# Optimization experiments

Hardware: AMD Instinct MI355X
Metric: run time of the kernel (lower is better)

## Reference

```python
import jax, jax.numpy as jnp
import numpy as np

B, C, H, W = 8, 512, 32, 32
NH = 8
DH = C // NH
HW = H * W
LN_EPS = 1e-5
NORM_EPS = 1e-12  # torch F.normalize eps


def setup_inputs() -> dict:
    key = jax.random.key(0)
    ks = jax.random.split(key, 8)
    s = 0.02
    return {
        "x": jax.random.normal(ks[0], (B, C, H, W), dtype=jnp.float32),
        "qkv_w": jax.random.normal(ks[1], (3 * C, C), dtype=jnp.float32) * s,
        "proj_w": jax.random.normal(ks[2], (C, C), dtype=jnp.float32) * s,
        "proj_b": jnp.zeros((C,), dtype=jnp.float32),
        "temperature": jnp.ones((NH, 1, 1), dtype=jnp.float32),
        "ln_g": jnp.ones((C,), dtype=jnp.float32),
        "ln_b": jnp.zeros((C,), dtype=jnp.float32),
        "pos_embed": jax.random.normal(ks[3], (1, HW, C), dtype=jnp.float32) * s,
        "dw_w": jax.random.normal(ks[4], (C, 1, 3, 3), dtype=jnp.float32) * s,
        "dw_b": jnp.zeros((C,), dtype=jnp.float32),
        "pw_w": jax.random.normal(ks[5], (C, C, 1, 1), dtype=jnp.float32) * s,
        "pw_b": jnp.zeros((C,), dtype=jnp.float32),
    }


def _l2norm_tokens(t):
    # normalize along token axis (dim=-2), like F.normalize(t, dim=-2)
    n = jnp.sqrt(jnp.sum(t * t, axis=-2, keepdims=True))
    return t / jnp.maximum(n, NORM_EPS)


def _layernorm(t, g, b):
    mu = jnp.mean(t, axis=-1, keepdims=True)
    var = jnp.mean((t - mu) ** 2, axis=-1, keepdims=True)
    return (t - mu) * jax.lax.rsqrt(var + LN_EPS) * g + b


def _dsconv(t, dw_w, dw_b, pw_w, pw_b):
    # depthwise 3x3 SAME + pointwise 1x1, NCHW / OIHW
    y = jax.lax.conv_general_dilated(
        t, dw_w, window_strides=(1, 1), padding="SAME",
        dimension_numbers=("NCHW", "OIHW", "NCHW"), feature_group_count=C)
    y = y + dw_b[None, :, None, None]
    y = jax.lax.conv_general_dilated(
        y, pw_w, window_strides=(1, 1), padding="SAME",
        dimension_numbers=("NCHW", "OIHW", "NCHW"))
    return y + pw_b[None, :, None, None]


def reference(x, qkv_w, proj_w, proj_b, temperature, ln_g, ln_b, pos_embed, dw_w, dw_b, pw_w, pw_b):
    save = x
    t = jnp.transpose(x.reshape(B, C, HW), (0, 2, 1))  # [B, HW, C]
    t = t + pos_embed
    # qkv projection (no bias)
    qkv = t @ qkv_w.T  # [B, HW, 3C]
    qkv = qkv.reshape(B, HW, 3, NH, DH).transpose(2, 0, 3, 1, 4)  # [3,B,NH,HW,DH]
    q, k, v = qkv[0], qkv[1], qkv[2]
    q = _l2norm_tokens(q)
    k = _l2norm_tokens(k)
    attn = jnp.einsum("bhnd,bhmd->bhnm", q, k) * temperature[None]  # [B,NH,HW,HW]
    attn = jax.nn.softmax(attn, axis=-1)
    o = jnp.einsum("bhnm,bhmd->bhnd", attn, v)  # [B,NH,HW,DH]
    o = o.transpose(0, 2, 1, 3).reshape(B, HW, C)
    o = o @ proj_w.T + proj_b
    o = _layernorm(o, ln_g, ln_b)
    o = jnp.transpose(o, (0, 2, 1)).reshape(B, C, H, W)
    o = o + save
    return o + _dsconv(o, dw_w, dw_b, pw_w, pw_b)
```

## Files before the change

### kernel.cpp

```cpp
#include <hip/hip_runtime.h>
#include <math.h>

#define BB_ 8
#define C_ 512
#define C3_ 1536
#define HW_ 1024
#define NH_ 8
#define DH_ 64
#define HH_ 32
#define WW_ 32

typedef __attribute__((ext_vector_type(8))) short short8;
typedef __attribute__((ext_vector_type(4))) short short4v;
typedef __attribute__((ext_vector_type(8))) unsigned short ushort8;
typedef __attribute__((ext_vector_type(4))) unsigned short ushort4_t;
typedef __attribute__((ext_vector_type(4))) float f32x4;
typedef unsigned short ushort;

__device__ inline ushort f2bf(float f) {
  union { float f; unsigned u; } v;
  v.f = f;
  unsigned r = v.u + 0x7fffu + ((v.u >> 16) & 1u);
  return (ushort)(r >> 16);
}
__device__ inline float bf2f(ushort u) {
  union { unsigned u; float f; } v;
  v.u = ((unsigned)u) << 16;
  return v.f;
}

__device__ inline float fast_exp2(float x) {
#if __has_builtin(__builtin_amdgcn_exp2f)
  return __builtin_amdgcn_exp2f(x);
#else
  return exp2f(x);
#endif
}

#define GLD16(gptr, lptr)                                                     \
  __builtin_amdgcn_global_load_lds(                                           \
      (const __attribute__((address_space(1))) unsigned int*)(gptr),          \
      (__attribute__((address_space(3))) unsigned int*)(lptr), 16, 0, 0)

__device__ inline f32x4 pv_mfma(short4v vf, short4v pf, f32x4 acc) {
#if __has_builtin(__builtin_amdgcn_mfma_f32_16x16x16_bf16)
  return __builtin_amdgcn_mfma_f32_16x16x16_bf16(vf, pf, acc, 0, 0, 0);
#elif __has_builtin(__builtin_amdgcn_mfma_f32_16x16x16bf16_1k)
  return __builtin_amdgcn_mfma_f32_16x16x16bf16_1k(vf, pf, acc, 0, 0, 0);
#else
  short8 vf8 = {vf[0], vf[1], vf[2], vf[3], 0, 0, 0, 0};
  short8 pf8 = {pf[0], pf[1], pf[2], pf[3], 0, 0, 0, 0};
  return __builtin_amdgcn_mfma_f32_16x16x32_bf16(vf8, pf8, acc, 0, 0, 0);
#endif
}

__global__ __launch_bounds__(256) void prep_kernel(
    const float* __restrict__ x, const float* __restrict__ pos,
    const float* __restrict__ qkv_w, const float* __restrict__ proj_w,
    const float* __restrict__ pw_w, ushort* __restrict__ t,
    ushort* __restrict__ xT, ushort* __restrict__ wts,
    float* __restrict__ sums) {
  const int bid = blockIdx.x;
  const int tid = threadIdx.x;
  if (bid >= 6144) {
    sums[(bid - 6144) * 256 + tid] = 0.f;
    return;
  }
  if (bid >= 1024) {
    int i = (bid - 1024) * 256 + tid;
    if (i < 786432) wts[i] = f2bf(qkv_w[i]);
    else if (i < 1048576) wts[i] = f2bf(proj_w[i - 786432]);
    else wts[i] = f2bf(pw_w[i - 1048576]);
    return;
  }
  __shared__ float tile[64][65];
  const int n0 = (bid & 15) * 64, c0 = ((bid >> 4) & 7) * 64, b = bid >> 7;
#pragma unroll
  for (int it = 0; it < 4; it++) {
    int c_l = (tid >> 4) + it * 16;
    int n_l4 = (tid & 15) * 4;
    float4 v = *(const float4*)&x[((size_t)(b * C_ + c0 + c_l)) * HW_ + n0 + n_l4];
    tile[c_l][n_l4 + 0] = v.x;
    tile[c_l][n_l4 + 1] = v.y;
    tile[c_l][n_l4 + 2] = v.z;
    tile[c_l][n_l4 + 3] = v.w;
  }
  __syncthreads();
#pragma unroll
  for (int it = 0; it < 4; it++) {
    int n_l = (tid >> 4) + it * 16;
    int c_l4 = (tid & 15) * 4;
    size_t token = (size_t)(b * HW_ + n0 + n_l);
    float4 pv = *(const float4*)&pos[(n0 + n_l) * C_ + c0 + c_l4];
    float xv0 = tile[c_l4 + 0][n_l], xv1 = tile[c_l4 + 1][n_l];
    float xv2 = tile[c_l4 + 2][n_l], xv3 = tile[c_l4 + 3][n_l];
    ushort4_t tb = {f2bf(xv0 + pv.x), f2bf(xv1 + pv.y), f2bf(xv2 + pv.z),
                    f2bf(xv3 + pv.w)};
    ushort4_t xb = {f2bf(xv0), f2bf(xv1), f2bf(xv2), f2bf(xv3)};
    *(ushort4_t*)&t[token * C_ + c0 + c_l4] = tb;
    *(ushort4_t*)&xT[token * C_ + c0 + c_l4] = xb;
  }
}

__global__ __launch_bounds__(256) void gemm_qkv(
    const ushort* __restrict__ A, const ushort* __restrict__ Wm,
    ushort* __restrict__ out, ushort* __restrict__ vt,
    float* __restrict__ qsum, float* __restrict__ ksum) {
  const int N = C3_, K = C_;
  __shared__ alignas(16) ushort As[128 * 32];
  __shared__ alignas(16) ushort Bs[128 * 32];
  const int bn = blockIdx.x * 128, bm = blockIdx.y * 128;
  const int tid = threadIdx.x;
  const int w = tid >> 6, lane = tid & 63;
  const int wm = 64 * (w & 1), wn = 64 * (w >> 1);
  const int l15 = lane & 15, lq = lane >> 4;

  f32x4 acc[4][4];
#pragma unroll
  for (int i = 0; i < 4; i++)
#pragma unroll
    for (int j = 0; j < 4; j++) acc[i][j] = (f32x4){0.f, 0.f, 0.f, 0.f};

  const int srr = lane >> 2, sq1 = lane & 3;

  for (int k0 = 0; k0 < K; k0 += 32) {
    __syncthreads();
#pragma unroll
    for (int j = 0; j < 2; j++) {
      int r = 32 * w + 16 * j + srr;
      int q = (sq1 - (r >> 1)) & 3;
      GLD16(A + (size_t)(bm + r) * K + k0 + q * 8, &As[(32 * w + 16 * j) * 32]);
      GLD16(Wm + (size_t)(bn + r) * K + k0 + q * 8, &Bs[(32 * w + 16 * j) * 32]);
    }
    __syncthreads();
    short8 af[4], bf[4];
#pragma unroll
    for (int nt = 0; nt < 4; nt++) {
      int r = wm + nt * 16 + l15;
      af[nt] = *(const short8*)&As[r * 32 + (((lq + (r >> 1)) & 3) * 8)];
      int c = wn + nt * 16 + l15;
      bf[nt] = *(const short8*)&Bs[c * 32 + (((lq + (c >> 1)) & 3) * 8)];
    }
#pragma unroll
    for (int i = 0; i < 4; i++)
#pragma unroll
      for (int j = 0; j < 4; j++)
        acc[i][j] = __builtin_amdgcn_mfma_f32_16x16x32_bf16(af[i], bf[j],
                                                            acc[i][j], 0, 0, 0);
  }

  const int b = bm >> 10;
  if (bn < 1024) {
#pragma unroll
    for (int j = 0; j < 4; j++) {
      int c = bn + wn + j * 16 + l15;
      float ss = 0.f;
#pragma unroll
      for (int i = 0; i < 4; i++) {
#pragma unroll
        for (int r = 0; r < 4; r++) {
          int m = bm + wm + i * 16 + lq * 4 + r;
          float v = acc[i][j][r];
          ss += v * v;
          out[(size_t)m * N + c] = f2bf(v);
        }
      }
      ss += __shfl_xor(ss, 16);
      ss += __shfl_xor(ss, 32);
      if (lq == 0) {
        if (c < 512) atomicAdd(&qsum[b * 512 + c], ss);
        else atomicAdd(&ksum[b * 512 + c - 512], ss);
      }
    }
  } else {
#pragma unroll
    for (int j = 0; j < 4; j++) {
      int c = bn + wn + j * 16 + l15;
      int hd = c - 1024;
      ushort* vrow = vt + ((size_t)(b * 512 + hd)) * HW_;
#pragma unroll
      for (int i = 0; i < 4; i++) {
        int n0 = (bm & 1023) + wm + i * 16 + lq * 4;
        ushort4_t pv = {f2bf(acc[i][j][0]), f2bf(acc[i][j][1]),
                        f2bf(acc[i][j][2]), f2bf(acc[i][j][3])};
        *(ushort4_t*)&vrow[n0] = pv;
      }
    }
  }
}

template <int EPI>
__global__ __launch_bounds__(256) void gemm_n64(
    const ushort* __restrict__ A, const ushort* __restrict__ Wm,
    const float* __restrict__ bias, void* __restrict__ outv,
    const ushort* __restrict__ resid, int N, int K) {
  __shared__ alignas(16) ushort As[128 * 32];
  __shared__ alignas(16) ushort Bs[64 * 32];
  __shared__ alignas(16) float Cs[EPI == 2 ? 64 * 128 : 4];
  const int bn = blockIdx.x * 64, bm = blockIdx.y * 128;
  const int tid = threadIdx.x;
  const int w = tid >> 6, lane = tid & 63;
  const int wm = 64 * (w & 1), wn = 32 * (w >> 1);
  const int l15 = lane & 15, lq = lane >> 4;

  f32x4 acc[4][2];
#pragma unroll
  for (int i = 0; i < 4; i++)
#pragma unroll
    for (int j = 0; j < 2; j++) acc[i][j] = (f32x4){0.f, 0.f, 0.f, 0.f};

  const int srr = lane >> 2, sq1 = lane & 3;

  for (int k0 = 0; k0 < K; k0 += 32) {
    __syncthreads();
#pragma unroll
    for (int j = 0; j < 2; j++) {
      int r = 32 * w + 16 * j + srr;
      int q = (sq1 - (r >> 1)) & 3;
      GLD16(A + (size_t)(bm + r) * K + k0 + q * 8, &As[(32 * w + 16 * j) * 32]);
    }
    {
      int r = 16 * w + srr;
      int q = (sq1 - (r >> 1)) & 3;
      GLD16(Wm + (size_t)(bn + r) * K + k0 + q * 8, &Bs[(16 * w) * 32]);
    }
    __syncthreads();
    short8 af[4], bf[2];
#pragma unroll
    for (int nt = 0; nt < 4; nt++) {
      int r = wm + nt * 16 + l15;
      af[nt] = *(const short8*)&As[r * 32 + (((lq + (r >> 1)) & 3) * 8)];
    }
#pragma unroll
    for (int j = 0; j < 2; j++) {
      int c = wn + j * 16 + l15;
      bf[j] = *(const short8*)&Bs[c * 32 + (((lq + (c >> 1)) & 3) * 8)];
    }
#pragma unroll
    for (int i = 0; i < 4; i++)
#pragma unroll
      for (int j = 0; j < 2; j++)
        acc[i][j] = __builtin_amdgcn_mfma_f32_16x16x32_bf16(af[i], bf[j],
                                                            acc[i][j], 0, 0, 0);
  }

  if (EPI == 1) {
#pragma unroll
    for (int i = 0; i < 4; i++) {
#pragma unroll
      for (int j = 0; j < 2; j++) {
        int c = bn + wn + j * 16 + l15;
        float bv = bias[c];
#pragma unroll
        for (int r = 0; r < 4; r++) {
          int m = bm + wm + i * 16 + lq * 4 + r;
          float v = acc[i][j][r] + bv;
          ((ushort*)outv)[(size_t)m * N + c] = f2bf(v);
        }
      }
    }
  } else {
#pragma unroll
    for (int i = 0; i < 4; i++) {
#pragma unroll
      for (int j = 0; j < 2; j++) {
        int c_l = wn + j * 16 + l15;
        int m_l = wm + i * 16 + lq * 4;
        float bv = bias[bn + c_l];
        f32x4 vv;
#pragma unroll
        for (int r = 0; r < 4; r++) {
          int m = bm + m_l + r;
          vv[r] = acc[i][j][r] + bv + bf2f(resid[(size_t)m * C_ + bn + c_l]);
        }
        int phys = (m_l >> 2) ^ (c_l & 31);
        *(f32x4*)&Cs[c_l * 128 + phys * 4] = vv;
      }
    }
    __syncthreads();
    const int b = bm >> 10, s0 = bm & (HW_ - 1);
    const int l5 = tid & 31;
    const int rr = tid >> 5;
    float* outp = (float*)outv;
#pragma unroll
    for (int pass = 0; pass < 8; pass++) {
      int row = rr + pass * 8;
      int phys = l5 ^ (row & 31);
      f32x4 vv = *(const f32x4*)&Cs[row * 128 + phys * 4];
      *(f32x4*)&outp[((size_t)(b * C_ + bn + row)) * HW_ + s0 + l5 * 4] = vv;
    }
  }
}

__global__ __launch_bounds__(256) void attn_mfma_kernel(
    const ushort* __restrict__ qkv, const ushort* __restrict__ vt,
    const float* __restrict__ qsum, const float* __restrict__ ksum,
    const float* __restrict__ temp, ushort* __restrict__ o) {
  __shared__ alignas(16) ushort Ks[2][64 * 64];
  __shared__ alignas(16) ushort Vts[2][64 * 64];
  __shared__ float sc_lds[64];

  const int tid = threadIdx.x;
  const int w = tid >> 6, lane = tid & 63;
  const int quad = lane >> 4, lcol = lane & 15;
  const int bh = blockIdx.x & 63;
  const int qt = blockIdx.x >> 6;
  const int b = bh >> 3, h = bh & 7;
  const int q0 = qt * 128;

  if (tid < 64) {
    float qs = qsum[b * 512 + h * 64 + tid];
    float ks = ksum[b * 512 + h * 64 + tid];
    float iq = 1.0f / fmaxf(sqrtf(qs), 1e-12f);
    float ik = 1.0f / fmaxf(sqrtf(ks), 1e-12f);
    sc_lds[tid] = iq * ik * temp[h] * 1.44269504088896340736f;
  }

  const ushort* kg = qkv + (size_t)b * HW_ * C3_ + C_ + h * 64;
  const ushort* vg = vt + (size_t)(bh * 64) * HW_;

  const int srow0 = tid >> 3;
  const int sc = tid & 7;

#pragma unroll
  for (int it = 0; it < 2; it++) {
    int row = srow0 + it * 32;
    int scg = sc ^ (row & 7);
    GLD16(kg + (size_t)row * C3_ + scg * 8, &Ks[0][w * 512 + it * 2048]);
    GLD16(vg + (size_t)row * HW_ + scg * 8, &Vts[0][w * 512 + it * 2048]);
  }
  __syncthreads();

  short8 qf[2][2];
#pragma unroll
  for (int qg = 0; qg < 2; qg++) {
    const int m = q0 + w * 32 + qg * 16 + lcol;
    const ushort* qrow = qkv + ((size_t)(b * HW_ + m)) * C3_ + h * 64;
#pragma unroll
    for (int kc = 0; kc < 2; kc++) {
      ushort8 q8 = *(const ushort8*)&qrow[kc * 32 + quad * 8];
      union { short8 v; ushort u[8]; } pk;
#pragma unroll
      for (int j = 0; j < 8; j++) {
        int d = kc * 32 + quad * 8 + j;
        pk.u[j] = f2bf(bf2f(q8[j]) * sc_lds[d]);
      }
      qf[qg][kc] = pk.v;
    }
  }

  f32x4 ot[2][4];
#pragma unroll
  for (int qg = 0; qg < 2; qg++)
#pragma unroll
    for (int dt = 0; dt < 4; dt++) ot[qg][dt] = (f32x4){0.f, 0.f, 0.f, 0.f};
  float lsum[2] = {0.f, 0.f};

  for (int kt = 0; kt < 16; kt++) {
    if (kt > 0) __syncthreads();
    const int cur = kt & 1;
    if (kt + 1 < 16) {
      const int nxt = cur ^ 1;
#pragma unroll
      for (int it = 0; it < 2; it++) {
        int row = srow0 + it * 32;
        int scg = sc ^ (row & 7);
        GLD16(kg + (size_t)((kt + 1) * 64 + row) * C3_ + scg * 8,
              &Ks[nxt][w * 512 + it * 2048]);
        GLD16(vg + (size_t)row * HW_ + (kt + 1) * 64 + scg * 8,
              &Vts[nxt][w * 512 + it * 2048]);
      }
    }

    f32x4 sfr[2][4];
#pragma unroll
    for (int qg = 0; qg < 2; qg++)
#pragma unroll
      for (int nt = 0; nt < 4; nt++) sfr[qg][nt] = (f32x4){0.f, 0.f, 0.f, 0.f};
#pragma unroll
    for (int kc = 0; kc < 2; kc++) {
#pragma unroll
      for (int nt = 0; nt < 4; nt++) {
        int row = nt * 16 + lcol;
        short8 kf = *(const short8*)
            &Ks[cur][row * 64 + (((kc * 4 + quad) ^ (row & 7)) * 8)];
        sfr[0][nt] = __builtin_amdgcn_mfma_f32_16x16x32_bf16(kf, qf[0][kc],
                                                             sfr[0][nt], 0, 0, 0);
        sfr[1][nt] = __builtin_amdgcn_mfma_f32_16x16x32_bf16(kf, qf[1][kc],
                                                             sfr[1][nt], 0, 0, 0);
      }
    }

    short4v pk[2][4];
#pragma unroll
    for (int qg = 0; qg < 2; qg++) {
#pragma unroll
      for (int nt = 0; nt < 4; nt++) {
        float f0 = fast_exp2(sfr[qg][nt][0]);
        float f1 = fast_exp2(sfr[qg][nt][1]);
        float f2 = fast_exp2(sfr[qg][nt][2]);
        float f3 = fast_exp2(sfr[qg][nt][3]);
        lsum[qg] += f0 + f1 + f2 + f3;
        pk[qg][nt] = (short4v){(short)f2bf(f0), (short)f2bf(f1),
                               (short)f2bf(f2), (short)f2bf(f3)};
      }
    }

#pragma unroll
    for (int nt = 0; nt < 4; nt++) {
      int key = nt * 16 + quad * 4;
#pragma unroll
      for (int dt = 0; dt < 4; dt++) {
        int d = dt * 16 + lcol;
        short4v vf = *(const short4v*)
            &Vts[cur][d * 64 + (((key >> 3) ^ (d & 7)) * 8) + (key & 7)];
        ot[0][dt] = pv_mfma(vf, pk[0][nt], ot[0][dt]);
        ot[1][dt] = pv_mfma(vf, pk[1][nt], ot[1][dt]);
      }
    }
  }

#pragma unroll
  for (int qg = 0; qg < 2; qg++) {
    float s = lsum[qg];
    s += __shfl_xor(s, 16);
    s += __shfl_xor(s, 32);
    const float inv = 1.0f / s;
    const int m = q0 + w * 32 + qg * 16 + lcol;
    ushort* orow = o + ((size_t)(b * HW_ + m)) * C_ + h * 64;
#pragma unroll
    for (int dt = 0; dt < 4; dt++) {
      ushort4_t pkb = {f2bf(ot[qg][dt][0] * inv), f2bf(ot[qg][dt][1] * inv),
                       f2bf(ot[qg][dt][2] * inv), f2bf(ot[qg][dt][3] * inv)};
      *(ushort4_t*)&orow[dt * 16 + quad * 4] = pkb;
    }
  }
}

__global__ __launch_bounds__(256) void ln_residual_kernel(
    const ushort* __restrict__ po, const ushort* xT,
    const float* __restrict__ g, const float* __restrict__ bb, ushort* ybf) {
  const int wv = threadIdx.x >> 6, lane = threadIdx.x & 63;
  const int token = blockIdx.x * 4 + wv;
  const int c0 = lane * 8;
  ushort8 p8 = *(const ushort8*)&po[(size_t)token * C_ + c0];
  float v[8];
  float s = 0.f;
#pragma unroll
  for (int j = 0; j < 8; j++) {
    v[j] = bf2f(p8[j]);
    s += v[j];
  }
#pragma unroll
  for (int off = 32; off; off >>= 1) s += __shfl_xor(s, off);
  float mu = s * (1.0f / C_);
  float vs = 0.f;
#pragma unroll
  for (int j = 0; j < 8; j++) {
    v[j] -= mu;
    vs += v[j] * v[j];
  }
#pragma unroll
  for (int off = 32; off; off >>= 1) vs += __shfl_xor(vs, off);
  float rstd = rsqrtf(vs * (1.0f / C_) + 1e-5f);
  float4 g0 = *(const float4*)&g[c0], g1 = *(const float4*)&g[c0 + 4];
  float4 b0 = *(const float4*)&bb[c0], b1 = *(const float4*)&bb[c0 + 4];
  ushort8 r8 = *(const ushort8*)&xT[(size_t)token * C_ + c0];
  float gg[8] = {g0.x, g0.y, g0.z, g0.w, g1.x, g1.y, g1.z, g1.w};
  float bbv[8] = {b0.x, b0.y, b0.z, b0.w, b1.x, b1.y, b1.z, b1.w};
  ushort8 pk;
#pragma unroll
  for (int j = 0; j < 8; j++)
    pk[j] = f2bf(v[j] * rstd * gg[j] + bbv[j] + bf2f(r8[j]));
  *(ushort8*)&ybf[(size_t)token * C_ + c0] = pk;
}

__global__ __launch_bounds__(256) void dwconv_kernel(
    const ushort* __restrict__ y, const float* __restrict__ w,
    const float* __restrict__ bias, ushort* __restrict__ out) {
  const int cg = threadIdx.x & 63, tg = threadIdx.x >> 6;
  const int c0 = cg * 8;
  float wreg[9][8], breg[8];
#pragma unroll
  for (int j = 0; j < 8; j++) {
    breg[j] = bias[c0 + j];
#pragma unroll
    for (int kk = 0; kk < 9; kk++) wreg[kk][j] = w[(c0 + j) * 9 + kk];
  }
  for (int i = 0; i < 4; i++) {
    int token = blockIdx.x * 16 + tg * 4 + i;
    int b = token >> 10, s = token & (HW_ - 1);
    int hh = s >> 5, ww = s & 31;
    float acc[8];
#pragma unroll
    for (int j = 0; j < 8; j++) acc[j] = breg[j];
#pragma unroll
    for (int ky = 0; ky < 3; ky++) {
      int yy = hh + ky - 1;
      if (yy < 0 || yy >= HH_) continue;
#pragma unroll
      for (int kx = 0; kx < 3; kx++) {
        int xx = ww + kx - 1;
        if (xx < 0 || xx >= WW_) continue;
        ushort8 v8 = *(const ushort8*)
            &y[((size_t)(b * HW_ + yy * 32 + xx)) * C_ + c0];
        const float* wk = wreg[ky * 3 + kx];
#pragma unroll
        for (int j = 0; j < 8; j++) acc[j] += wk[j] * bf2f(v8[j]);
      }
    }
    ushort8 pk;
#pragma unroll
    for (int j = 0; j < 8; j++) pk[j] = f2bf(acc[j]);
    *(ushort8*)&out[(size_t)token * C_ + c0] = pk;
  }
}

extern "C" void kernel_launch(void* const* d_in, const int* in_sizes, int n_in,
                              void* d_out, int out_size, void* d_ws,
                              size_t ws_size, hipStream_t stream) {
  const float* x = (const float*)d_in[0];
  const float* qkv_w = (const float*)d_in[1];
  const float* proj_w = (const float*)d_in[2];
  const float* proj_b = (const float*)d_in[3];
  const float* temperature = (const float*)d_in[4];
  const float* ln_g = (const float*)d_in[5];
  const float* ln_b = (const float*)d_in[6];
  const float* pos = (const float*)d_in[7];
  const float* dw_w = (const float*)d_in[8];
  const float* dw_b = (const float*)d_in[9];
  const float* pw_w = (const float*)d_in[10];
  const float* pw_b = (const float*)d_in[11];
  float* out = (float*)d_out;

  float* ws = (float*)d_ws;
  ushort* qkv_bf = (ushort*)ws;
  ushort* t_bf = (ushort*)(ws + (size_t)6 * 1024 * 1024);
  ushort* proj_bf = (ushort*)(ws + (size_t)8 * 1024 * 1024);
  ushort* xT_bf = (ushort*)(ws + (size_t)12 * 1024 * 1024);
  ushort* wts = (ushort*)(ws + (size_t)14 * 1024 * 1024);
  ushort* qkvw_bf = wts;
  ushort* projw_bf = wts + 786432;
  ushort* pww_bf = wts + 1048576;
  float* sums = ws + (size_t)15 * 1024 * 1024;
  float* qsum = sums;
  float* ksum = sums + 4096;
  ushort* vtb = (ushort*)(ws + (size_t)16 * 1024 * 1024);

  const int M = BB_ * HW_;

  prep_kernel<<<6176, 256, 0, stream>>>(x, pos, qkv_w, proj_w, pw_w, t_bf,
                                        xT_bf, wts, sums);
  gemm_qkv<<<dim3(C3_ / 128, M / 128), 256, 0, stream>>>(
      t_bf, qkvw_bf, qkv_bf, vtb, qsum, ksum);
  attn_mfma_kernel<<<BB_ * NH_ * (HW_ / 128), 256, 0, stream>>>(
      qkv_bf, vtb, qsum, ksum, temperature, t_bf);
  gemm_n64<1><<<dim3(C_ / 64, M / 128), 256, 0, stream>>>(
      t_bf, projw_bf, proj_b, proj_bf, nullptr, C_, C_);
  ln_residual_kernel<<<M / 4, 256, 0, stream>>>(proj_bf, xT_bf, ln_g, ln_b,
                                                xT_bf);
  dwconv_kernel<<<M / 16, 256, 0, stream>>>(xT_bf, dw_w, dw_b, t_bf);
  gemm_n64<2><<<dim3(C_ / 64, M / 128), 256, 0, stream>>>(
      t_bf, pww_bf, pw_b, out, xT_bf, C_, C_);
}
```

Before: 200.2 us.

## Fuse projection GEMM with LayerNorm and residual; use packed bf16 converts

Replaces the separate projection GEMM and LayerNorm+residual kernels with one kernel in which each 512-thread block computes full 512-column rows for 32 tokens, then does the row reduction in registers and shared memory before writing the normalized output plus residual. This removes the round trip of the bf16 projection intermediate and one launch. The weight conversion in prep is vectorized to four elements per thread, and scalar bf16 rounding is swapped for the hardware packed-convert instruction throughout. In exchange, every block re-streams the whole 512x512 weight, the grid is smaller, the final stores are scalar 2-byte writes, and variance is computed as E[x^2]-mu^2.

```diff
diff --git a/kernel.cpp b/kernel.cpp
--- a/kernel.cpp
+++ b/kernel.cpp
@@ -27,6 +27,12 @@
   union { unsigned u; float f; } v;
   v.u = ((unsigned)u) << 16;
   return v.f;
+}
+
+__device__ inline unsigned cvt_pk_bf16(float a, float b) {
+  unsigned r;
+  asm("v_cvt_pk_bf16_f32 %0, %1, %2" : "=v"(r) : "v"(a), "v"(b));
+  return r;
 }
 
 __device__ inline float fast_exp2(float x) {
@@ -62,15 +68,20 @@
     float* __restrict__ sums) {
   const int bid = blockIdx.x;
   const int tid = threadIdx.x;
-  if (bid >= 6144) {
-    sums[(bid - 6144) * 256 + tid] = 0.f;
+  if (bid >= 2304) {
+    sums[(bid - 2304) * 256 + tid] = 0.f;
     return;
   }
   if (bid >= 1024) {
-    int i = (bid - 1024) * 256 + tid;
-    if (i < 786432) wts[i] = f2bf(qkv_w[i]);
-    else if (i < 1048576) wts[i] = f2bf(proj_w[i - 786432]);
-    else wts[i] = f2bf(pw_w[i - 1048576]);
+    int i = ((bid - 1024) * 256 + tid) * 4;
+    float4 v;
+    if (i < 786432) v = *(const float4*)&qkv_w[i];
+    else if (i < 1048576) v = *(const float4*)&proj_w[i - 786432];
+    else v = *(const float4*)&pw_w[i - 1048576];
+    union { unsigned u[2]; ushort4_t s; } o4;
+    o4.u[0] = cvt_pk_bf16(v.x, v.y);
+    o4.u[1] = cvt_pk_bf16(v.z, v.w);
+    *(ushort4_t*)&wts[i] = o4.s;
     return;
   }
   __shared__ float tile[64][65];
@@ -181,9 +192,10 @@
 #pragma unroll
       for (int i = 0; i < 4; i++) {
         int n0 = (bm & 1023) + wm + i * 16 + lq * 4;
-        ushort4_t pv = {f2bf(acc[i][j][0]), f2bf(acc[i][j][1]),
-                        f2bf(acc[i][j][2]), f2bf(acc[i][j][3])};
-        *(ushort4_t*)&vrow[n0] = pv;
+        union { unsigned u[2]; ushort4_t s; } pu;
+        pu.u[0] = cvt_pk_bf16(acc[i][j][0], acc[i][j][1]);
+        pu.u[1] = cvt_pk_bf16(acc[i][j][2], acc[i][j][3]);
+        *(ushort4_t*)&vrow[n0] = pu.s;
       }
     }
   }
@@ -401,8 +413,10 @@
         float f2 = fast_exp2(sfr[qg][nt][2]);
         float f3 = fast_exp2(sfr[qg][nt][3]);
         lsum[qg] += f0 + f1 + f2 + f3;
-        pk[qg][nt] = (short4v){(short)f2bf(f0), (short)f2bf(f1),
-                               (short)f2bf(f2), (short)f2bf(f3)};
+        union { unsigned u[2]; short4v s; } uu;
+        uu.u[0] = cvt_pk_bf16(f0, f1);
+        uu.u[1] = cvt_pk_bf16(f2, f3);
+        pk[qg][nt] = uu.s;
       }
     }
 
@@ -430,49 +444,150 @@
     ushort* orow = o + ((size_t)(b * HW_ + m)) * C_ + h * 64;
 #pragma unroll
     for (int dt = 0; dt < 4; dt++) {
-      ushort4_t pkb = {f2bf(ot[qg][dt][0] * inv), f2bf(ot[qg][dt][1] * inv),
-                       f2bf(ot[qg][dt][2] * inv), f2bf(ot[qg][dt][3] * inv)};
-      *(ushort4_t*)&orow[dt * 16 + quad * 4] = pkb;
-    }
-  }
-}
-
-__global__ __launch_bounds__(256) void ln_residual_kernel(
-    const ushort* __restrict__ po, const ushort* xT,
-    const float* __restrict__ g, const float* __restrict__ bb, ushort* ybf) {
-  const int wv = threadIdx.x >> 6, lane = threadIdx.x & 63;
-  const int token = blockIdx.x * 4 + wv;
-  const int c0 = lane * 8;
-  ushort8 p8 = *(const ushort8*)&po[(size_t)token * C_ + c0];
-  float v[8];
-  float s = 0.f;
-#pragma unroll
-  for (int j = 0; j < 8; j++) {
-    v[j] = bf2f(p8[j]);
-    s += v[j];
-  }
-#pragma unroll
-  for (int off = 32; off; off >>= 1) s += __shfl_xor(s, off);
-  float mu = s * (1.0f / C_);
-  float vs = 0.f;
-#pragma unroll
-  for (int j = 0; j < 8; j++) {
-    v[j] -= mu;
-    vs += v[j] * v[j];
-  }
-#pragma unroll
-  for (int off = 32; off; off >>= 1) vs += __shfl_xor(vs, off);
-  float rstd = rsqrtf(vs * (1.0f / C_) + 1e-5f);
-  float4 g0 = *(const float4*)&g[c0], g1 = *(const float4*)&g[c0 + 4];
-  float4 b0 = *(const float4*)&bb[c0], b1 = *(const float4*)&bb[c0 + 4];
-  ushort8 r8 = *(const ushort8*)&xT[(size_t)token * C_ + c0];
-  float gg[8] = {g0.x, g0.y, g0.z, g0.w, g1.x, g1.y, g1.z, g1.w};
-  float bbv[8] = {b0.x, b0.y, b0.z, b0.w, b1.x, b1.y, b1.z, b1.w};
-  ushort8 pk;
-#pragma unroll
-  for (int j = 0; j < 8; j++)
-    pk[j] = f2bf(v[j] * rstd * gg[j] + bbv[j] + bf2f(r8[j]));
-  *(ushort8*)&ybf[(size_t)token * C_ + c0] = pk;
+      union { unsigned u[2]; ushort4_t s4; } pu;
+      pu.u[0] = cvt_pk_bf16(ot[qg][dt][0] * inv, ot[qg][dt][1] * inv);
+      pu.u[1] = cvt_pk_bf16(ot[qg][dt][2] * inv, ot[qg][dt][3] * inv);
+      *(ushort4_t*)&orow[dt * 16 + quad * 4] = pu.s4;
+    }
+  }
+}
+
+__global__ __launch_bounds__(512) void gemm_proj_ln(
+    const ushort* __restrict__ A, const ushort* __restrict__ Wm,
+    const float* __restrict__ bias, const float* __restrict__ g,
+    const float* __restrict__ bb, const ushort* __restrict__ resid,
+    ushort* __restrict__ ybf) {
+  __shared__ alignas(16) ushort As[2][32 * 32];
+  __shared__ alignas(16) ushort Bs[2][512 * 32];
+  __shared__ float red[8][32][2];
+  const int bm = blockIdx.x * 32;
+  const int tid = threadIdx.x;
+  const int w = tid >> 6, lane = tid & 63;
+  const int l15 = lane & 15, lq = lane >> 4;
+  const int srr = lane >> 2, sq1 = lane & 3;
+
+  f32x4 acc[2][4];
+#pragma unroll
+  for (int i = 0; i < 2; i++)
+#pragma unroll
+    for (int j = 0; j < 4; j++) acc[i][j] = (f32x4){0.f, 0.f, 0.f, 0.f};
+
+  auto stage = [&](int kt, int bufi) {
+#pragma unroll
+    for (int it = 0; it < 4; it++) {
+      int r = it * 128 + w * 16 + srr;
+      int q = (sq1 - (r >> 1)) & 3;
+      GLD16(Wm + (size_t)r * C_ + kt * 32 + q * 8,
+            &Bs[bufi][(it * 128 + w * 16) * 32]);
+    }
+    if (w < 2) {
+      int r = w * 16 + srr;
+      int q = (sq1 - (r >> 1)) & 3;
+      GLD16(A + (size_t)(bm + r) * C_ + kt * 32 + q * 8,
+            &As[bufi][(w * 16) * 32]);
+    }
+  };
+
+  stage(0, 0);
+
+  for (int ks = 0; ks < 16; ks++) {
+    __syncthreads();
+    const int cur = ks & 1;
+    if (ks + 1 < 16) stage(ks + 1, cur ^ 1);
+
+    short8 af[2], bf[4];
+#pragma unroll
+    for (int i = 0; i < 2; i++) {
+      int r = i * 16 + l15;
+      af[i] = *(const short8*)&As[cur][r * 32 + (((lq + (r >> 1)) & 3) * 8)];
+    }
+#pragma unroll
+    for (int j = 0; j < 4; j++) {
+      int c = w * 64 + j * 16 + l15;
+      bf[j] = *(const short8*)&Bs[cur][c * 32 + (((lq + (c >> 1)) & 3) * 8)];
+    }
+#pragma unroll
+    for (int i = 0; i < 2; i++)
+#pragma unroll
+      for (int j = 0; j < 4; j++)
+        acc[i][j] = __builtin_amdgcn_mfma_f32_16x16x32_bf16(af[i], bf[j],
+                                                            acc[i][j], 0, 0, 0);
+  }
+
+  float bv[4];
+#pragma unroll
+  for (int j = 0; j < 4; j++) bv[j] = bias[w * 64 + j * 16 + l15];
+
+  float s1v[2][4], s2v[2][4];
+#pragma unroll
+  for (int i = 0; i < 2; i++) {
+#pragma unroll
+    for (int r = 0; r < 4; r++) {
+      float a = 0.f, q2 = 0.f;
+#pragma unroll
+      for (int j = 0; j < 4; j++) {
+        float v = acc[i][j][r] + bv[j];
+        acc[i][j][r] = v;
+        a += v;
+        q2 += v * v;
+      }
+      s1v[i][r] = a;
+      s2v[i][r] = q2;
+    }
+  }
+#pragma unroll
+  for (int off = 1; off < 16; off <<= 1) {
+#pragma unroll
+    for (int i = 0; i < 2; i++)
+#pragma unroll
+      for (int r = 0; r < 4; r++) {
+        s1v[i][r] += __shfl_xor(s1v[i][r], off);
+        s2v[i][r] += __shfl_xor(s2v[i][r], off);
+      }
+  }
+  if (l15 == 0) {
+#pragma unroll
+    for (int i = 0; i < 2; i++)
+#pragma unroll
+      for (int r = 0; r < 4; r++) {
+        int tok = i * 16 + lq * 4 + r;
+        red[w][tok][0] = s1v[i][r];
+        red[w][tok][1] = s2v[i][r];
+      }
+  }
+  __syncthreads();
+
+  float gv[4], bbv[4];
+#pragma unroll
+  for (int j = 0; j < 4; j++) {
+    gv[j] = g[w * 64 + j * 16 + l15];
+    bbv[j] = bb[w * 64 + j * 16 + l15];
+  }
+
+#pragma unroll
+  for (int i = 0; i < 2; i++) {
+#pragma unroll
+    for (int r = 0; r < 4; r++) {
+      int tok = i * 16 + lq * 4 + r;
+      float su = 0.f, sq = 0.f;
+#pragma unroll
+      for (int ww = 0; ww < 8; ww++) {
+        su += red[ww][tok][0];
+        sq += red[ww][tok][1];
+      }
+      float mu = su * (1.0f / C_);
+      float var = sq * (1.0f / C_) - mu * mu;
+      float rstd = rsqrtf(var + 1e-5f);
+      int m = bm + tok;
+#pragma unroll
+      for (int j = 0; j < 4; j++) {
+        int c = w * 64 + j * 16 + l15;
+        float y = (acc[i][j][r] - mu) * rstd * gv[j] + bbv[j] +
+                  bf2f(resid[(size_t)m * C_ + c]);
+        ybf[(size_t)m * C_ + c] = f2bf(y);
+      }
+    }
+  }
 }
 
 __global__ __launch_bounds__(256) void dwconv_kernel(
@@ -509,10 +624,12 @@
         for (int j = 0; j < 8; j++) acc[j] += wk[j] * bf2f(v8[j]);
       }
     }
-    ushort8 pk;
-#pragma unroll
-    for (int j = 0; j < 8; j++) pk[j] = f2bf(acc[j]);
-    *(ushort8*)&out[(size_t)token * C_ + c0] = pk;
+    union { unsigned u[4]; ushort8 v; } pku;
+    pku.u[0] = cvt_pk_bf16(acc[0], acc[1]);
+    pku.u[1] = cvt_pk_bf16(acc[2], acc[3]);
+    pku.u[2] = cvt_pk_bf16(acc[4], acc[5]);
+    pku.u[3] = cvt_pk_bf16(acc[6], acc[7]);
+    *(ushort8*)&out[(size_t)token * C_ + c0] = pku.v;
   }
 }
 
@@ -536,7 +653,6 @@
   float* ws = (float*)d_ws;
   ushort* qkv_bf = (ushort*)ws;
   ushort* t_bf = (ushort*)(ws + (size_t)6 * 1024 * 1024);
-  ushort* proj_bf = (ushort*)(ws + (size_t)8 * 1024 * 1024);
   ushort* xT_bf = (ushort*)(ws + (size_t)12 * 1024 * 1024);
   ushort* wts = (ushort*)(ws + (size_t)14 * 1024 * 1024);
   ushort* qkvw_bf = wts;
@@ -549,16 +665,14 @@
 
   const int M = BB_ * HW_;
 
-  prep_kernel<<<6176, 256, 0, stream>>>(x, pos, qkv_w, proj_w, pw_w, t_bf,
+  prep_kernel<<<2336, 256, 0, stream>>>(x, pos, qkv_w, proj_w, pw_w, t_bf,
                                         xT_bf, wts, sums);
   gemm_qkv<<<dim3(C3_ / 128, M / 128), 256, 0, stream>>>(
       t_bf, qkvw_bf, qkv_bf, vtb, qsum, ksum);
   attn_mfma_kernel<<<BB_ * NH_ * (HW_ / 128), 256, 0, stream>>>(
       qkv_bf, vtb, qsum, ksum, temperature, t_bf);
-  gemm_n64<1><<<dim3(C_ / 64, M / 128), 256, 0, stream>>>(
-      t_bf, projw_bf, proj_b, proj_bf, nullptr, C_, C_);
-  ln_residual_kernel<<<M / 4, 256, 0, stream>>>(proj_bf, xT_bf, ln_g, ln_b,
-                                                xT_bf);
+  gemm_proj_ln<<<M / 32, 512, 0, stream>>>(t_bf, projw_bf, proj_b, ln_g,
+                                           ln_b, xT_bf, xT_bf);
   dwconv_kernel<<<M / 16, 256, 0, stream>>>(xT_bf, dw_w, dw_b, t_bf);
   gemm_n64<2><<<dim3(C_ / 64, M / 128), 256, 0, stream>>>(
       t_bf, pww_bf, pw_b, out, xT_bf, C_, C_);
```

Measured after the change: 200.0 us. Within noise of the previous version (-0.1%).
